# Kernel tuning notes

Hardware: AMD Instinct MI355X
Metric: run time of the kernel (lower is better)

Reference implementation:

```python
import jax, jax.numpy as jnp
import numpy as np

B, L, C = 4, 1024, 768
H = 12
D = C // H  # head_dim = 64


def setup_inputs() -> dict:
    key = jax.random.key(0)
    k_x, k_qkv, k_pw, k_pb = jax.random.split(key, 4)
    x = jax.random.normal(k_x, (B, L, C), dtype=jnp.float32)
    # torch nn.Linear(C, 3C, bias=False): weight [3C, C]
    w_qkv = jax.random.normal(k_qkv, (3 * C, C), dtype=jnp.float32) * (1.0 / np.sqrt(C))
    # torch nn.Linear(C, C): weight [C, C], bias [C]
    w_proj = jax.random.normal(k_pw, (C, C), dtype=jnp.float32) * (1.0 / np.sqrt(C))
    b_proj = jax.random.normal(k_pb, (C,), dtype=jnp.float32) * 0.01
    return {"x": x, "w_qkv": w_qkv, "w_proj": w_proj, "b_proj": b_proj}


def reference(x, w_qkv, w_proj, b_proj):
    scale = D ** (-0.5)
    # qkv: [B, L, 3C] -> [3, B, H, L, D]
    qkv = jnp.einsum('blc,fc->blf', x, w_qkv)
    qkv = qkv.reshape(B, L, 3, H, D).transpose(2, 0, 3, 1, 4)
    q, k, v = qkv[0], qkv[1], qkv[2]
    # attention scores [B, H, L, L], materialized (returned by the module)
    attn = jnp.einsum('bhld,bhmd->bhlm', q, k) * scale
    attn_score = jax.nn.softmax(attn, axis=-1)
    # dropout_p = 0.0 -> identity
    out = jnp.einsum('bhlm,bhmd->bhld', attn_score, v)
    out = out.transpose(0, 2, 1, 3).reshape(B, L, C)
    out = jnp.einsum('blc,fc->blf', out, w_proj) + b_proj
    return (out, attn_score)
```

## Files before the change

### kernel.cpp

```cpp
#include <hip/hip_runtime.h>
#include <hip/hip_bf16.h>
#include <stdint.h>


typedef __attribute__((ext_vector_type(8))) short short8;
typedef __attribute__((ext_vector_type(4))) float floatx4;

#define MFMA16(A_, B_, C_) __builtin_amdgcn_mfma_f32_16x16x32_bf16((A_), (B_), (C_), 0, 0, 0)

__device__ __forceinline__ unsigned short f2bf(float f) {
  unsigned u = __builtin_bit_cast(unsigned, f);
  u += 0x7FFFu + ((u >> 16) & 1u);
  return (unsigned short)(u >> 16);
}
__device__ __forceinline__ float bf2f(unsigned short u) {
  return __builtin_bit_cast(float, (unsigned)u << 16);
}

__global__ __launch_bounds__(256) void cast3_kernel(const float* __restrict__ x,
                                                    const float* __restrict__ wq,
                                                    const float* __restrict__ wp,
                                                    unsigned short* __restrict__ dst) {
  const int NX = 3145728, NWQ = 1769472;
  int i = (blockIdx.x * 256 + threadIdx.x) * 4;
  const float* src;
  int off;
  if (i < NX) { src = x; off = i; }
  else if (i < NX + NWQ) { src = wq; off = i - NX; }
  else { src = wp; off = i - NX - NWQ; }
  float4 v = *(const float4*)(src + off);
  ushort4 o;
  o.x = f2bf(v.x); o.y = f2bf(v.y); o.z = f2bf(v.z); o.w = f2bf(v.w);
  *(ushort4*)(dst + i) = o;
}

template <int EPI, int BN>
__global__ __launch_bounds__(256) void gemm_bt(
    const unsigned short* __restrict__ A, const unsigned short* __restrict__ Bm,
    const float* __restrict__ bias,
    unsigned short* __restrict__ q_ws, unsigned short* __restrict__ k_ws,
    unsigned short* __restrict__ vt_ws, float* __restrict__ Cout,
    int M, int N, int K) {
  constexpr int NJ = BN / 32;
  constexpr int QN = BN / 2;
  __shared__ __align__(16) unsigned short Al[2][128 * 32];
  __shared__ __align__(16) unsigned short Bl[2][BN * 32];
  const int tid = threadIdx.x;
  const int lane = tid & 63, wave = tid >> 6;
  const int q = lane >> 4, lm = lane & 15;
  const int wm = wave >> 1, wn = wave & 1;
  const int m0 = blockIdx.y * 128, n0 = blockIdx.x * BN;

  floatx4 acc[4][NJ];
#pragma unroll
  for (int i = 0; i < 4; ++i)
#pragma unroll
    for (int j = 0; j < NJ; ++j) acc[i][j] = (floatx4){0.f, 0.f, 0.f, 0.f};

  auto stage = [&](int k0, int buf) {
#pragma unroll
    for (int it = 0; it < 2; ++it) {
      int idx = tid + it * 256;
      int row = idx >> 2, ch = idx & 3;
      const unsigned short* ga = A + (size_t)(m0 + row) * K + k0 + ch * 8;
      __builtin_amdgcn_global_load_lds(
          (const __attribute__((address_space(1))) unsigned int*)ga,
          (__attribute__((address_space(3))) unsigned int*)(&Al[buf][0] + idx * 8), 16, 0, 0);
    }
#pragma unroll
    for (int it = 0; it < BN / 64; ++it) {
      int idx = tid + it * 256;
      int row = idx >> 2, ch = idx & 3;
      const unsigned short* gb = Bm + (size_t)(n0 + row) * K + k0 + ch * 8;
      __builtin_amdgcn_global_load_lds(
          (const __attribute__((address_space(1))) unsigned int*)gb,
          (__attribute__((address_space(3))) unsigned int*)(&Bl[buf][0] + idx * 8), 16, 0, 0);
    }
  };

  stage(0, 0);
  __syncthreads();
  int cur = 0;
  for (int k0 = 0; k0 < K; k0 += 32) {
    if (k0 + 32 < K) stage(k0 + 32, cur ^ 1);
    short8 af[4], bfr[NJ];
#pragma unroll
    for (int t = 0; t < 4; ++t)
      af[t] = *(const short8*)(&Al[cur][0] + (wm * 64 + t * 16 + lm) * 32 + q * 8);
#pragma unroll
    for (int t = 0; t < NJ; ++t)
      bfr[t] = *(const short8*)(&Bl[cur][0] + (wn * QN + t * 16 + lm) * 32 + q * 8);
#pragma unroll
    for (int i = 0; i < 4; ++i)
#pragma unroll
      for (int j = 0; j < NJ; ++j) acc[i][j] = MFMA16(af[i], bfr[j], acc[i][j]);
    __syncthreads();
    cur ^= 1;
  }

  if (EPI == 0) {
#pragma unroll
    for (int i = 0; i < 4; ++i) {
      int mb = m0 + wm * 64 + i * 16 + q * 4;
#pragma unroll
      for (int j = 0; j < NJ; ++j) {
        int n = n0 + wn * QN + j * 16 + lm;
        int which = n / 768;
        int r = n - which * 768;
        int h = r >> 6, d = r & 63;
        if (which == 2) {
          int b = mb >> 10, l = mb & 1023;
          ushort4 pk;
          pk.x = f2bf(acc[i][j][0]);
          pk.y = f2bf(acc[i][j][1]);
          pk.z = f2bf(acc[i][j][2]);
          pk.w = f2bf(acc[i][j][3]);
          *(ushort4*)(vt_ws + (size_t)((b * 12 + h) * 64 + d) * 1024 + l) = pk;
        } else {
          unsigned short* dst = (which == 0) ? q_ws : k_ws;
          float sc = (which == 0) ? 0.125f : 1.0f;
#pragma unroll
          for (int rg = 0; rg < 4; ++rg) {
            int m = mb + rg;
            int b = m >> 10, l = m & 1023;
            dst[(size_t)((b * 12 + h) * 1024 + l) * 64 + d] = f2bf(acc[i][j][rg] * sc);
          }
        }
      }
    }
  } else {
#pragma unroll
    for (int i = 0; i < 4; ++i) {
      int mb = m0 + wm * 64 + i * 16 + q * 4;
#pragma unroll
      for (int j = 0; j < NJ; ++j) {
        int n = n0 + wn * QN + j * 16 + lm;
        float bv = bias[n];
#pragma unroll
        for (int rg = 0; rg < 4; ++rg) {
          int m = mb + rg;
          Cout[(size_t)m * N + n] = acc[i][j][rg] + bv;
        }
      }
    }
  }
}

__global__ __launch_bounds__(256) void attn_mfma(
    const unsigned short* __restrict__ q_ws, const unsigned short* __restrict__ k_ws,
    const unsigned short* __restrict__ vt_ws, unsigned short* __restrict__ attn_o,
    float* __restrict__ out1) {
  constexpr int L = 1024, SW = 1032;
  constexpr float LOG2E = 1.44269504f;
  __shared__ __align__(16) unsigned short S[16 * SW];
  __shared__ float stats[2][4][16];
  const int flat = blockIdx.x;
  const int swz = (flat & 7) * 384 + (flat >> 3);
  const int bh = swz >> 6, b = bh / 12, h = bh % 12;
  const int l0 = (swz & 63) * 16;
  const int tid = threadIdx.x, lane = tid & 63, wave = tid >> 6;
  const int q = lane >> 4, lm = lane & 15;

  const size_t qk_base = (size_t)bh * L * 64;

  const unsigned short* qr = q_ws + qk_base + (size_t)(l0 + lm) * 64;
  short8 bq0 = *(const short8*)(qr + q * 8);
  short8 bq1 = *(const short8*)(qr + 32 + q * 8);

  floatx4 acc[16];
  __builtin_amdgcn_s_setprio(1);
#pragma unroll
  for (int ct = 0; ct < 16; ++ct) {
    const unsigned short* kr = k_ws + qk_base + (size_t)((wave * 16 + ct) * 16 + lm) * 64;
    short8 a0 = *(const short8*)(kr + q * 8);
    short8 a1 = *(const short8*)(kr + 32 + q * 8);
    floatx4 c = (floatx4){0.f, 0.f, 0.f, 0.f};
    c = MFMA16(a0, bq0, c);
    c = MFMA16(a1, bq1, c);
    acc[ct] = c;
  }
  __builtin_amdgcn_s_setprio(0);

  float mloc = -1e30f;
#pragma unroll
  for (int ct = 0; ct < 16; ++ct)
#pragma unroll
    for (int rg = 0; rg < 4; ++rg) mloc = fmaxf(mloc, acc[ct][rg]);
  mloc = fmaxf(mloc, __shfl_xor(mloc, 16));
  mloc = fmaxf(mloc, __shfl_xor(mloc, 32));

  float ssum = 0.f;
#pragma unroll
  for (int ct = 0; ct < 16; ++ct) {
#pragma unroll
    for (int rg = 0; rg < 4; ++rg) {
      float e = exp2f((acc[ct][rg] - mloc) * LOG2E);
      acc[ct][rg] = e;
      ssum += e;
    }
  }
  ssum += __shfl_xor(ssum, 16);
  ssum += __shfl_xor(ssum, 32);
  if (lane < 16) {
    stats[0][wave][lane] = mloc;
    stats[1][wave][lane] = ssum;
  }
  __syncthreads();

  float m0_ = stats[0][0][lm], m1_ = stats[0][1][lm];
  float m2_ = stats[0][2][lm], m3_ = stats[0][3][lm];
  float m = fmaxf(fmaxf(m0_, m1_), fmaxf(m2_, m3_));
  float sum = stats[1][0][lm] * exp2f((m0_ - m) * LOG2E)
            + stats[1][1][lm] * exp2f((m1_ - m) * LOG2E)
            + stats[1][2][lm] * exp2f((m2_ - m) * LOG2E)
            + stats[1][3][lm] * exp2f((m3_ - m) * LOG2E);
  float wscale = exp2f((mloc - m) * LOG2E) / sum;

  float* orow = out1 + (size_t)bh * L * L + (size_t)(l0 + lm) * L + wave * 256 + q * 4;
  unsigned short* srow = S + lm * SW + wave * 256 + q * 4;
#pragma unroll
  for (int ct = 0; ct < 16; ++ct) {
    float p0 = acc[ct][0] * wscale, p1 = acc[ct][1] * wscale;
    float p2 = acc[ct][2] * wscale, p3 = acc[ct][3] * wscale;
    ushort4 pk;
    pk.x = f2bf(p0); pk.y = f2bf(p1); pk.z = f2bf(p2); pk.w = f2bf(p3);
    *(ushort4*)(srow + ct * 16) = pk;
    float4 pv;
    pv.x = p0; pv.y = p1; pv.z = p2; pv.w = p3;
    *(float4*)(orow + ct * 16) = pv;
  }
  __syncthreads();

  {
    floatx4 pacc = (floatx4){0.f, 0.f, 0.f, 0.f};
    const unsigned short* vr = vt_ws + (size_t)(bh * 64 + wave * 16 + lm) * 1024;
    __builtin_amdgcn_s_setprio(1);
#pragma unroll 4
    for (int ks = 0; ks < 32; ++ks) {
      short8 af = *(const short8*)(S + lm * SW + ks * 32 + q * 8);
      short8 bv = *(const short8*)(vr + ks * 32 + q * 8);
      pacc = MFMA16(af, bv, pacc);
    }
    __builtin_amdgcn_s_setprio(0);
#pragma unroll
    for (int rg = 0; rg < 4; ++rg) {
      int row = q * 4 + rg;
      attn_o[(size_t)(b * 1024 + l0 + row) * 768 + h * 64 + wave * 16 + lm] = f2bf(pacc[rg]);
    }
  }
}

extern "C" void kernel_launch(void* const* d_in, const int* in_sizes, int n_in,
                              void* d_out, int out_size, void* d_ws, size_t ws_size,
                              hipStream_t stream) {
  const float* x      = (const float*)d_in[0];
  const float* w_qkv  = (const float*)d_in[1];
  const float* w_proj = (const float*)d_in[2];
  const float* b_proj = (const float*)d_in[3];

  float* out0 = (float*)d_out;
  float* out1 = out0 + (size_t)4096 * 768;

  const size_t NX = (size_t)4096 * 768;
  const size_t NWQ = (size_t)2304 * 768;
  const size_t NWP = (size_t)768 * 768;
  const size_t NQ = (size_t)48 * 1024 * 64;

  unsigned short* x_bf   = (unsigned short*)d_ws;
  unsigned short* wq_bf  = x_bf + NX;
  unsigned short* wp_bf  = wq_bf + NWQ;
  unsigned short* q_ws   = wp_bf + NWP;
  unsigned short* k_ws   = q_ws + NQ;
  unsigned short* vt_ws  = k_ws + NQ;
  unsigned short* attn_o = vt_ws + NQ;

  cast3_kernel<<<dim3((NX + NWQ + NWP) / 1024), dim3(256), 0, stream>>>(x, w_qkv, w_proj, x_bf);

  gemm_bt<0, 128><<<dim3(2304 / 128, 4096 / 128), dim3(256), 0, stream>>>(
      x_bf, wq_bf, nullptr, q_ws, k_ws, vt_ws, nullptr, 4096, 2304, 768);

  attn_mfma<<<dim3(3072), dim3(256), 0, stream>>>(q_ws, k_ws, vt_ws, attn_o, out1);

  gemm_bt<1, 64><<<dim3(768 / 64, 4096 / 128), dim3(256), 0, stream>>>(
      attn_o, wp_bf, b_proj, nullptr, nullptr, nullptr, out0, 4096, 768, 768);
}
```

Baseline: 339.0 us.

## Widen attention blocks to 32 rows, swizzle GEMM grids, use nontemporal stores

```diff
diff --git a/kernel.cpp b/kernel.cpp
--- a/kernel.cpp
+++ b/kernel.cpp
@@ -40,7 +40,7 @@
     const float* __restrict__ bias,
     unsigned short* __restrict__ q_ws, unsigned short* __restrict__ k_ws,
     unsigned short* __restrict__ vt_ws, float* __restrict__ Cout,
-    int M, int N, int K) {
+    int M, int N, int K, int nbx, int chunk) {
   constexpr int NJ = BN / 32;
   constexpr int QN = BN / 2;
   __shared__ __align__(16) unsigned short Al[2][128 * 32];
@@ -49,7 +49,9 @@
   const int lane = tid & 63, wave = tid >> 6;
   const int q = lane >> 4, lm = lane & 15;
   const int wm = wave >> 1, wn = wave & 1;
-  const int m0 = blockIdx.y * 128, n0 = blockIdx.x * BN;
+  const int flat = blockIdx.x;
+  const int swz = (flat & 7) * chunk + (flat >> 3);
+  const int m0 = (swz / nbx) * 128, n0 = (swz % nbx) * BN;
 
   floatx4 acc[4][NJ];
 #pragma unroll
@@ -139,31 +141,33 @@
 #pragma unroll
         for (int rg = 0; rg < 4; ++rg) {
           int m = mb + rg;
-          Cout[(size_t)m * N + n] = acc[i][j][rg] + bv;
+          __builtin_nontemporal_store(acc[i][j][rg] + bv, Cout + (size_t)m * N + n);
         }
       }
     }
   }
 }
 
-__global__ __launch_bounds__(256) void attn_mfma(
+__global__ __launch_bounds__(512, 4) void attn_mfma(
     const unsigned short* __restrict__ q_ws, const unsigned short* __restrict__ k_ws,
     const unsigned short* __restrict__ vt_ws, unsigned short* __restrict__ attn_o,
     float* __restrict__ out1) {
   constexpr int L = 1024, SW = 1032;
   constexpr float LOG2E = 1.44269504f;
-  __shared__ __align__(16) unsigned short S[16 * SW];
-  __shared__ float stats[2][4][16];
+  __shared__ __align__(16) unsigned short S[32 * SW];
+  __shared__ float stats[2][8][16];
   const int flat = blockIdx.x;
-  const int swz = (flat & 7) * 384 + (flat >> 3);
-  const int bh = swz >> 6, b = bh / 12, h = bh % 12;
-  const int l0 = (swz & 63) * 16;
+  const int swz = (flat & 7) * 192 + (flat >> 3);
+  const int bh = swz >> 5, b = bh / 12, h = bh % 12;
+  const int l0 = (swz & 31) * 32;
   const int tid = threadIdx.x, lane = tid & 63, wave = tid >> 6;
   const int q = lane >> 4, lm = lane & 15;
+  const int rowgrp = wave >> 2, w4 = wave & 3;
+  const int qrow = l0 + rowgrp * 16 + lm;
 
   const size_t qk_base = (size_t)bh * L * 64;
 
-  const unsigned short* qr = q_ws + qk_base + (size_t)(l0 + lm) * 64;
+  const unsigned short* qr = q_ws + qk_base + (size_t)qrow * 64;
   short8 bq0 = *(const short8*)(qr + q * 8);
   short8 bq1 = *(const short8*)(qr + 32 + q * 8);
 
@@ -171,7 +175,7 @@
   __builtin_amdgcn_s_setprio(1);
 #pragma unroll
   for (int ct = 0; ct < 16; ++ct) {
-    const unsigned short* kr = k_ws + qk_base + (size_t)((wave * 16 + ct) * 16 + lm) * 64;
+    const unsigned short* kr = k_ws + qk_base + (size_t)((w4 * 16 + ct) * 16 + lm) * 64;
     short8 a0 = *(const short8*)(kr + q * 8);
     short8 a1 = *(const short8*)(kr + 32 + q * 8);
     floatx4 c = (floatx4){0.f, 0.f, 0.f, 0.f};
@@ -207,17 +211,18 @@
   }
   __syncthreads();
 
-  float m0_ = stats[0][0][lm], m1_ = stats[0][1][lm];
-  float m2_ = stats[0][2][lm], m3_ = stats[0][3][lm];
+  const int wb = rowgrp * 4;
+  float m0_ = stats[0][wb + 0][lm], m1_ = stats[0][wb + 1][lm];
+  float m2_ = stats[0][wb + 2][lm], m3_ = stats[0][wb + 3][lm];
   float m = fmaxf(fmaxf(m0_, m1_), fmaxf(m2_, m3_));
-  float sum = stats[1][0][lm] * exp2f((m0_ - m) * LOG2E)
-            + stats[1][1][lm] * exp2f((m1_ - m) * LOG2E)
-            + stats[1][2][lm] * exp2f((m2_ - m) * LOG2E)
-            + stats[1][3][lm] * exp2f((m3_ - m) * LOG2E);
+  float sum = stats[1][wb + 0][lm] * exp2f((m0_ - m) * LOG2E)
+            + stats[1][wb + 1][lm] * exp2f((m1_ - m) * LOG2E)
+            + stats[1][wb + 2][lm] * exp2f((m2_ - m) * LOG2E)
+            + stats[1][wb + 3][lm] * exp2f((m3_ - m) * LOG2E);
   float wscale = exp2f((mloc - m) * LOG2E) / sum;
 
-  float* orow = out1 + (size_t)bh * L * L + (size_t)(l0 + lm) * L + wave * 256 + q * 4;
-  unsigned short* srow = S + lm * SW + wave * 256 + q * 4;
+  float* orow = out1 + (size_t)bh * L * L + (size_t)qrow * L + w4 * 256 + q * 4;
+  unsigned short* srow = S + (rowgrp * 16 + lm) * SW + w4 * 256 + q * 4;
 #pragma unroll
   for (int ct = 0; ct < 16; ++ct) {
     float p0 = acc[ct][0] * wscale, p1 = acc[ct][1] * wscale;
@@ -225,27 +230,27 @@
     ushort4 pk;
     pk.x = f2bf(p0); pk.y = f2bf(p1); pk.z = f2bf(p2); pk.w = f2bf(p3);
     *(ushort4*)(srow + ct * 16) = pk;
-    float4 pv;
-    pv.x = p0; pv.y = p1; pv.z = p2; pv.w = p3;
-    *(float4*)(orow + ct * 16) = pv;
+    floatx4 pv = (floatx4){p0, p1, p2, p3};
+    __builtin_nontemporal_store(pv, (floatx4*)(orow + ct * 16));
   }
   __syncthreads();
 
   {
     floatx4 pacc = (floatx4){0.f, 0.f, 0.f, 0.f};
-    const unsigned short* vr = vt_ws + (size_t)(bh * 64 + wave * 16 + lm) * 1024;
+    const unsigned short* vr = vt_ws + (size_t)(bh * 64 + w4 * 16 + lm) * 1024;
+    const unsigned short* sbase = S + (rowgrp * 16 + lm) * SW;
     __builtin_amdgcn_s_setprio(1);
 #pragma unroll 4
     for (int ks = 0; ks < 32; ++ks) {
-      short8 af = *(const short8*)(S + lm * SW + ks * 32 + q * 8);
+      short8 af = *(const short8*)(sbase + ks * 32 + q * 8);
       short8 bv = *(const short8*)(vr + ks * 32 + q * 8);
       pacc = MFMA16(af, bv, pacc);
     }
     __builtin_amdgcn_s_setprio(0);
 #pragma unroll
     for (int rg = 0; rg < 4; ++rg) {
-      int row = q * 4 + rg;
-      attn_o[(size_t)(b * 1024 + l0 + row) * 768 + h * 64 + wave * 16 + lm] = f2bf(pacc[rg]);
+      int row = rowgrp * 16 + q * 4 + rg;
+      attn_o[(size_t)(b * 1024 + l0 + row) * 768 + h * 64 + w4 * 16 + lm] = f2bf(pacc[rg]);
     }
   }
 }
@@ -276,11 +281,11 @@
 
   cast3_kernel<<<dim3((NX + NWQ + NWP) / 1024), dim3(256), 0, stream>>>(x, w_qkv, w_proj, x_bf);
 
-  gemm_bt<0, 128><<<dim3(2304 / 128, 4096 / 128), dim3(256), 0, stream>>>(
-      x_bf, wq_bf, nullptr, q_ws, k_ws, vt_ws, nullptr, 4096, 2304, 768);
-
-  attn_mfma<<<dim3(3072), dim3(256), 0, stream>>>(q_ws, k_ws, vt_ws, attn_o, out1);
-
-  gemm_bt<1, 64><<<dim3(768 / 64, 4096 / 128), dim3(256), 0, stream>>>(
-      attn_o, wp_bf, b_proj, nullptr, nullptr, nullptr, out0, 4096, 768, 768);
-}
+  gemm_bt<0, 128><<<dim3(576), dim3(256), 0, stream>>>(
+      x_bf, wq_bf, nullptr, q_ws, k_ws, vt_ws, nullptr, 4096, 2304, 768, 18, 72);
+
+  attn_mfma<<<dim3(1536), dim3(512), 0, stream>>>(q_ws, k_ws, vt_ws, attn_o, out1);
+
+  gemm_bt<1, 64><<<dim3(384), dim3(256), 0, stream>>>(
+      attn_o, wp_bf, b_proj, nullptr, nullptr, nullptr, out0, 4096, 768, 768, 12, 48);
+}
```

Result: slower. 346.5 us (+2.2%).
